# Kernel tuning notes

Hardware: AMD Instinct MI355X
Metric: run time of the kernel (lower is better)

The kernel has to match this reference:

```python
import jax, jax.numpy as jnp
import numpy as np

EPS_GAUSS = 1e-15
EPS_SOFTMAX = 1e-16

N, F, M, K = 200000, 256, 128, 8
ATT = 128
NUM_GRAPHS = 1024


def setup_inputs() -> dict:
    key = jax.random.key(0)
    ks = jax.random.split(key, 7)
    x = jax.random.normal(ks[0], (N, F), dtype=jnp.float32)
    # glorot-ish scales keep pre-gaussian activations in a sane range
    g = jax.random.normal(ks[1], (F, K * M), dtype=jnp.float32) * 0.05
    mu = jax.random.normal(ks[2], (K, M), dtype=jnp.float32) * 0.1
    sigma = jax.random.normal(ks[3], (K, M), dtype=jnp.float32) * 0.1
    w1 = jax.random.normal(ks[4], (ATT, M), dtype=jnp.float32) * 0.09
    w2 = jax.random.normal(ks[5], (1, ATT), dtype=jnp.float32) * 0.1
    batch = jnp.sort(jax.random.randint(ks[6], (N,), 0, NUM_GRAPHS, dtype=jnp.int64))
    return {"x": x, "g": g, "mu": mu, "sigma": sigma, "w1": w1,
            "w2": w2, "batch": batch, "num_graphs": NUM_GRAPHS}


def reference(x, g, mu, sigma, w1, w2, batch, num_graphs):
    n = x.shape[0]
    k, m = mu.shape
    # GMM "conv": dense matmul then Gaussian-mixture elementwise chain
    out = (x @ g).reshape(n, k, m)                       # [N, K, M]
    gauss = jnp.exp(-0.5 * (out - mu[None]) ** 2 / (EPS_GAUSS + sigma[None] ** 2))
    H = jnp.sum(out * gauss, axis=1)                     # [N, M]
    # attention pooling: scores per node
    a = jnp.tanh(H @ w1.T)                               # [N, ATT] (b1 unused in source)
    scores = a @ w2.T                                    # [N, 1]
    # segment (per-graph) softmax
    smax = jax.ops.segment_max(scores, batch, num_segments=num_graphs)
    e = jnp.exp(scores - smax[batch])
    ssum = jax.ops.segment_sum(e, batch, num_segments=num_graphs)
    S = e / (ssum[batch] + EPS_SOFTMAX)                  # [N, 1]
    # scatter_add pooling -> [num_graphs, M]
    return jax.ops.segment_sum(S * H, batch, num_segments=num_graphs)
```

## Files before the change

kernel.cpp:

```cpp
#include <hip/hip_runtime.h>
#include <hip/hip_bf16.h>
#include <hip/hip_fp16.h>
#include <math.h>

#define N_NODES 200000
#define FDIM    256
#define MDIM    128
#define KMIX    8
#define ATTD    128
#define NGRAPH  1024
#define TSN     64

typedef _Float16 half8 __attribute__((ext_vector_type(8)));
typedef _Float16 half4 __attribute__((ext_vector_type(4)));
typedef float    floatx4 __attribute__((ext_vector_type(4)));

__global__ __launch_bounds__(256) void pack_g(
    const float* __restrict__ g, _Float16* __restrict__ gh, _Float16* __restrict__ gl)
{
    int t    = blockIdx.x * 256 + threadIdx.x;
    int lane = t & 63;
    int frag = t >> 6;
    int fc   = frag & 7;
    int ctg  = (frag >> 3) & 7;
    int k    = frag >> 6;
    int col  = k * 128 + ctg * 16 + (lane & 15);
    int f0   = fc * 32 + (lane >> 4) * 8;
    half8 vh, vl;
    #pragma unroll
    for (int j = 0; j < 8; ++j) {
        float v = g[(size_t)(f0 + j) * 1024 + col];
        _Float16 h = (_Float16)v;
        vh[j] = h;
        vl[j] = (_Float16)(v - (float)h);
    }
    *(half8*)(gh + (size_t)t * 8) = vh;
    *(half8*)(gl + (size_t)t * 8) = vl;
}

__global__ __launch_bounds__(256) void pack_w1(
    const float* __restrict__ w1, _Float16* __restrict__ w1h, _Float16* __restrict__ w1l)
{
    int t    = blockIdx.x * 256 + threadIdx.x;
    int lane = t & 63;
    int frag = t >> 6;
    int mc   = frag & 3;
    int ctg  = frag >> 2;
    int att  = ctg * 16 + (lane & 15);
    int m0   = mc * 32 + (lane >> 4) * 8;
    half8 vh, vl;
    #pragma unroll
    for (int j = 0; j < 8; ++j) {
        float v = w1[att * MDIM + m0 + j];
        _Float16 h = (_Float16)v;
        vh[j] = h;
        vl[j] = (_Float16)(v - (float)h);
    }
    *(half8*)(w1h + (size_t)t * 8) = vh;
    *(half8*)(w1l + (size_t)t * 8) = vl;
}

__global__ __launch_bounds__(512, 4) void fused_forward(
    const float* __restrict__ x,
    const _Float16* __restrict__ gh, const _Float16* __restrict__ gl,
    const float* __restrict__ mu, const float* __restrict__ sigma,
    const _Float16* __restrict__ w1h, const _Float16* __restrict__ w1l,
    const float* __restrict__ w2,
    float* __restrict__ Hout, float* __restrict__ scores)
{
    __shared__ unsigned char smem[64 * 264 * 2 * 2];
    _Float16* xs_h = (_Float16*)smem;
    _Float16* xs_l = xs_h + 64 * 264;
    float*    Hs   = (float*)smem;
    float*    spart = (float*)(smem + 64 * 264 * 2);

    const int tid   = threadIdx.x;
    const int nBase = blockIdx.x * TSN;

    {
        const float4* xg = (const float4*)x;
        #pragma unroll
        for (int r = 0; r < 8; ++r) {
            int idx  = r * 512 + tid;
            int row  = idx >> 6;
            int quad = idx & 63;
            float4 v = xg[(size_t)(nBase + row) * 64 + quad];
            half4 h, l;
            h[0] = (_Float16)v.x; l[0] = (_Float16)(v.x - (float)h[0]);
            h[1] = (_Float16)v.y; l[1] = (_Float16)(v.y - (float)h[1]);
            h[2] = (_Float16)v.z; l[2] = (_Float16)(v.z - (float)h[2]);
            h[3] = (_Float16)v.w; l[3] = (_Float16)(v.w - (float)h[3]);
            *(half4*)&xs_h[row * 264 + quad * 4] = h;
            *(half4*)&xs_l[row * 264 + quad * 4] = l;
        }
    }
    __syncthreads();

    const int wave  = tid >> 6;
    const int lane  = tid & 63;
    const int c15   = lane & 15;
    const int q     = lane >> 4;
    const int nhalf = wave >> 2;
    const int colq  = wave & 3;

    float h[2][2][4];
    #pragma unroll
    for (int rt = 0; rt < 2; ++rt)
        #pragma unroll
        for (int ct = 0; ct < 2; ++ct)
            #pragma unroll
            for (int rg = 0; rg < 4; ++rg) h[rt][ct][rg] = 0.f;

    #pragma unroll 1
    for (int k = 0; k < KMIX; ++k) {
        floatx4 acc[2][2];
        #pragma unroll
        for (int rt = 0; rt < 2; ++rt)
            #pragma unroll
            for (int ct = 0; ct < 2; ++ct) acc[rt][ct] = (floatx4)0.f;

        #pragma unroll 2
        for (int fc = 0; fc < 8; ++fc) {
            const int f0 = fc * 32 + q * 8;
            half8 Ah[2], Al[2];
            #pragma unroll
            for (int rt = 0; rt < 2; ++rt) {
                int node = nhalf * 32 + rt * 16 + c15;
                Ah[rt] = *(const half8*)&xs_h[node * 264 + f0];
                Al[rt] = *(const half8*)&xs_l[node * 264 + f0];
            }
            half8 Bh[2], Bl[2];
            #pragma unroll
            for (int ct = 0; ct < 2; ++ct) {
                int ctg = colq * 2 + ct;
                size_t off = ((size_t)((k * 8 + ctg) * 8 + fc) * 64 + lane) * 8;
                Bh[ct] = *(const half8*)(gh + off);
                Bl[ct] = *(const half8*)(gl + off);
            }
            #pragma unroll
            for (int rt = 0; rt < 2; ++rt)
                #pragma unroll
                for (int ct = 0; ct < 2; ++ct) {
                    acc[rt][ct] = __builtin_amdgcn_mfma_f32_16x16x32_f16(Ah[rt], Bh[ct], acc[rt][ct], 0, 0, 0);
                    acc[rt][ct] = __builtin_amdgcn_mfma_f32_16x16x32_f16(Ah[rt], Bl[ct], acc[rt][ct], 0, 0, 0);
                    acc[rt][ct] = __builtin_amdgcn_mfma_f32_16x16x32_f16(Al[rt], Bh[ct], acc[rt][ct], 0, 0, 0);
                }
        }

        #pragma unroll
        for (int ct = 0; ct < 2; ++ct) {
            int col = k * 128 + colq * 32 + ct * 16 + c15;
            float muv = mu[col];
            float sg  = sigma[col];
            float iv  = 1.0f / (1e-15f + sg * sg);
            #pragma unroll
            for (int rt = 0; rt < 2; ++rt)
                #pragma unroll
                for (int rg = 0; rg < 4; ++rg) {
                    float o = acc[rt][ct][rg];
                    float d = o - muv;
                    h[rt][ct][rg] += o * __expf(-0.5f * d * d * iv);
                }
        }
    }

    __syncthreads();
    const int HS_LD = MDIM + 4;
    #pragma unroll
    for (int rt = 0; rt < 2; ++rt)
        #pragma unroll
        for (int ct = 0; ct < 2; ++ct)
            #pragma unroll
            for (int rg = 0; rg < 4; ++rg) {
                int n = nhalf * 32 + rt * 16 + q * 4 + rg;
                int m = colq * 32 + ct * 16 + c15;
                float v = h[rt][ct][rg];
                Hs[n * HS_LD + m] = v;
                Hout[(size_t)(nBase + n) * MDIM + m] = v;
            }
    __syncthreads();

    {
        floatx4 datt[2][2];
        #pragma unroll
        for (int rt = 0; rt < 2; ++rt)
            #pragma unroll
            for (int ct = 0; ct < 2; ++ct) datt[rt][ct] = (floatx4)0.f;

        #pragma unroll
        for (int mc = 0; mc < 4; ++mc) {
            half8 Ah[2], Al[2];
            #pragma unroll
            for (int rt = 0; rt < 2; ++rt) {
                int node = nhalf * 32 + rt * 16 + c15;
                const float* hp = &Hs[node * HS_LD + mc * 32 + q * 8];
                #pragma unroll
                for (int j = 0; j < 8; ++j) {
                    float v = hp[j];
                    _Float16 hi = (_Float16)v;
                    Ah[rt][j] = hi;
                    Al[rt][j] = (_Float16)(v - (float)hi);
                }
            }
            #pragma unroll
            for (int ct = 0; ct < 2; ++ct) {
                int frag = (colq * 2 + ct) * 4 + mc;
                size_t off = ((size_t)frag * 64 + lane) * 8;
                half8 Bh = *(const half8*)(w1h + off);
                half8 Bl = *(const half8*)(w1l + off);
                #pragma unroll
                for (int rt = 0; rt < 2; ++rt) {
                    datt[rt][ct] = __builtin_amdgcn_mfma_f32_16x16x32_f16(Ah[rt], Bh, datt[rt][ct], 0, 0, 0);
                    datt[rt][ct] = __builtin_amdgcn_mfma_f32_16x16x32_f16(Ah[rt], Bl, datt[rt][ct], 0, 0, 0);
                    datt[rt][ct] = __builtin_amdgcn_mfma_f32_16x16x32_f16(Al[rt], Bh, datt[rt][ct], 0, 0, 0);
                }
            }
        }

        float w2v[2];
        #pragma unroll
        for (int ct = 0; ct < 2; ++ct) w2v[ct] = w2[colq * 32 + ct * 16 + c15];

        #pragma unroll
        for (int rt = 0; rt < 2; ++rt) {
            #pragma unroll
            for (int rg = 0; rg < 4; ++rg) {
                float p = 0.f;
                #pragma unroll
                for (int ct = 0; ct < 2; ++ct) {
                    float dot = datt[rt][ct][rg];
                    float e2 = __expf(2.f * dot);
                    float av = 1.f - 2.f / (e2 + 1.f);
                    p = fmaf(av, w2v[ct], p);
                }
                p += __shfl_xor(p, 1);
                p += __shfl_xor(p, 2);
                p += __shfl_xor(p, 4);
                p += __shfl_xor(p, 8);
                if (c15 == 0) {
                    int n = nhalf * 32 + rt * 16 + q * 4 + rg;
                    spart[n * 4 + colq] = p;
                }
            }
        }
    }
    __syncthreads();
    if (tid < 64) {
        const float* sp = &spart[tid * 4];
        scores[nBase + tid] = (sp[0] + sp[1]) + (sp[2] + sp[3]);
    }
}

__global__ __launch_bounds__(256) void segment_pool(
    const float* __restrict__ H, const float* __restrict__ scores,
    const int* __restrict__ batch, float* __restrict__ out)
{
    const int gidx = blockIdx.x;
    const int tid  = threadIdx.x;

    int lo = 0, hi = N_NODES;
    while (lo < hi) { int mid = (lo + hi) >> 1; if (batch[mid] <  gidx) lo = mid + 1; else hi = mid; }
    const int start = lo;
    hi = N_NODES;
    while (lo < hi) { int mid = (lo + hi) >> 1; if (batch[mid] <= gidx) lo = mid + 1; else hi = mid; }
    const int end = lo;

    __shared__ float red[4];

    float mx = -INFINITY;
    for (int i = start + tid; i < end; i += 256) mx = fmaxf(mx, scores[i]);
    #pragma unroll
    for (int o = 32; o > 0; o >>= 1) mx = fmaxf(mx, __shfl_xor(mx, o));
    if ((tid & 63) == 0) red[tid >> 6] = mx;
    __syncthreads();
    mx = fmaxf(fmaxf(red[0], red[1]), fmaxf(red[2], red[3]));
    __syncthreads();

    float s = 0.f;
    for (int i = start + tid; i < end; i += 256) s += __expf(scores[i] - mx);
    #pragma unroll
    for (int o = 32; o > 0; o >>= 1) s += __shfl_xor(s, o);
    if ((tid & 63) == 0) red[tid >> 6] = s;
    __syncthreads();
    s = red[0] + red[1] + red[2] + red[3];
    const float inv = 1.f / (s + 1e-16f);

    const int m = tid & 127;
    const int p = tid >> 7;
    float acc = 0.f;
    for (int i = start + p; i < end; i += 2)
        acc = fmaf(__expf(scores[i] - mx), H[(size_t)i * MDIM + m], acc);
    __shared__ float part[2][128];
    part[p][m] = acc;
    __syncthreads();
    if (tid < 128) out[gidx * MDIM + tid] = (part[0][tid] + part[1][tid]) * inv;
}

extern "C" void kernel_launch(void* const* d_in, const int* in_sizes, int n_in,
                              void* d_out, int out_size, void* d_ws, size_t ws_size,
                              hipStream_t stream)
{
    const float* x     = (const float*)d_in[0];
    const float* g     = (const float*)d_in[1];
    const float* mu    = (const float*)d_in[2];
    const float* sigma = (const float*)d_in[3];
    const float* w1    = (const float*)d_in[4];
    const float* w2    = (const float*)d_in[5];
    const int*   batch = (const int*)d_in[6];
    float* out = (float*)d_out;

    float*    H      = (float*)d_ws;
    float*    scores = H + (size_t)N_NODES * MDIM;
    _Float16* ghp    = (_Float16*)(scores + N_NODES);
    _Float16* glp    = ghp + (size_t)FDIM * KMIX * MDIM;
    _Float16* w1hp   = glp + (size_t)FDIM * KMIX * MDIM;
    _Float16* w1lp   = w1hp + (size_t)ATTD * MDIM;

    pack_g<<<128, 256, 0, stream>>>(g, ghp, glp);
    pack_w1<<<8, 256, 0, stream>>>(w1, w1hp, w1lp);
    fused_forward<<<N_NODES / TSN, 512, 0, stream>>>(x, ghp, glp, mu, sigma,
                                                     w1hp, w1lp, w2, H, scores);
    segment_pool<<<NGRAPH, 256, 0, stream>>>(H, scores, batch, out);
}
```

Before: 680.9 us.

## Double-buffer GEMM operand loads, coalesce H stores, restructure segment pooling

The main GEMM loop now software-pipelines its LDS A-fragment and global B-fragment loads into double-buffered registers, prefetching the next k/fc step while the current MFMAs run. H is staged through shared memory and written to global with coalesced float4 stores instead of scattered scalar writes. The segment pooling kernel fuses the exp-sum pass with the weighted accumulation, caching exp values in shared-memory chunks and reading H as float4 across 8 node-parallel groups. This adds register pressure from the doubled operand buffers, which could hurt occupancy at launch bounds of 512 threads and 4 blocks.

```diff
diff --git a/kernel.cpp b/kernel.cpp
--- a/kernel.cpp
+++ b/kernel.cpp
@@ -68,11 +68,11 @@
     const float* __restrict__ w2,
     float* __restrict__ Hout, float* __restrict__ scores)
 {
-    __shared__ unsigned char smem[64 * 264 * 2 * 2];
+    __shared__ unsigned char smem[64 * 264 * 2 * 2 + 512];
     _Float16* xs_h = (_Float16*)smem;
     _Float16* xs_l = xs_h + 64 * 264;
     float*    Hs   = (float*)smem;
-    float*    spart = (float*)(smem + 64 * 264 * 2);
+    float*    spart = (float*)(smem + 64 * 264 * 2 * 2);
 
     const int tid   = threadIdx.x;
     const int nBase = blockIdx.x * TSN;
@@ -103,6 +103,9 @@
     const int nhalf = wave >> 2;
     const int colq  = wave & 3;
 
+    const _Float16* gh0 = gh + (size_t)(colq * 2) * 4096 + lane * 8;
+    const _Float16* gl0 = gl + (size_t)(colq * 2) * 4096 + lane * 8;
+
     float h[2][2][4];
     #pragma unroll
     for (int rt = 0; rt < 2; ++rt)
@@ -110,6 +113,31 @@
         for (int ct = 0; ct < 2; ++ct)
             #pragma unroll
             for (int rg = 0; rg < 4; ++rg) h[rt][ct][rg] = 0.f;
+
+    half8 Ah[2][2], Al[2][2], Bh[2][2], Bl[2][2];
+
+#define LOAD_A(buf, fcv)                                                      \
+    {                                                                         \
+        const int f0_ = (fcv) * 32 + q * 8;                                   \
+        _Pragma("unroll")                                                     \
+        for (int rt = 0; rt < 2; ++rt) {                                      \
+            int node_ = nhalf * 32 + rt * 16 + c15;                           \
+            Ah[buf][rt] = *(const half8*)&xs_h[node_ * 264 + f0_];            \
+            Al[buf][rt] = *(const half8*)&xs_l[node_ * 264 + f0_];            \
+        }                                                                     \
+    }
+#define LOAD_B(buf, kv, fcv)                                                  \
+    {                                                                         \
+        size_t o_ = (size_t)(kv) * 32768 + (size_t)(fcv) * 512;               \
+        _Pragma("unroll")                                                     \
+        for (int ct = 0; ct < 2; ++ct) {                                      \
+            Bh[buf][ct] = *(const half8*)(gh0 + o_ + ct * 4096);              \
+            Bl[buf][ct] = *(const half8*)(gl0 + o_ + ct * 4096);              \
+        }                                                                     \
+    }
+
+    LOAD_A(0, 0)
+    LOAD_B(0, 0, 0)
 
     #pragma unroll 1
     for (int k = 0; k < KMIX; ++k) {
@@ -119,31 +147,20 @@
             #pragma unroll
             for (int ct = 0; ct < 2; ++ct) acc[rt][ct] = (floatx4)0.f;
 
-        #pragma unroll 2
+        #pragma unroll
         for (int fc = 0; fc < 8; ++fc) {
-            const int f0 = fc * 32 + q * 8;
-            half8 Ah[2], Al[2];
-            #pragma unroll
-            for (int rt = 0; rt < 2; ++rt) {
-                int node = nhalf * 32 + rt * 16 + c15;
-                Ah[rt] = *(const half8*)&xs_h[node * 264 + f0];
-                Al[rt] = *(const half8*)&xs_l[node * 264 + f0];
-            }
-            half8 Bh[2], Bl[2];
-            #pragma unroll
-            for (int ct = 0; ct < 2; ++ct) {
-                int ctg = colq * 2 + ct;
-                size_t off = ((size_t)((k * 8 + ctg) * 8 + fc) * 64 + lane) * 8;
-                Bh[ct] = *(const half8*)(gh + off);
-                Bl[ct] = *(const half8*)(gl + off);
-            }
+            const int cur = fc & 1, nxt = cur ^ 1;
+            const int nfc = (fc + 1) & 7;
+            const int nk  = (fc == 7) ? ((k + 1) & 7) : k;
+            LOAD_A(nxt, nfc)
+            LOAD_B(nxt, nk, nfc)
             #pragma unroll
             for (int rt = 0; rt < 2; ++rt)
                 #pragma unroll
                 for (int ct = 0; ct < 2; ++ct) {
-                    acc[rt][ct] = __builtin_amdgcn_mfma_f32_16x16x32_f16(Ah[rt], Bh[ct], acc[rt][ct], 0, 0, 0);
-                    acc[rt][ct] = __builtin_amdgcn_mfma_f32_16x16x32_f16(Ah[rt], Bl[ct], acc[rt][ct], 0, 0, 0);
-                    acc[rt][ct] = __builtin_amdgcn_mfma_f32_16x16x32_f16(Al[rt], Bh[ct], acc[rt][ct], 0, 0, 0);
+                    acc[rt][ct] = __builtin_amdgcn_mfma_f32_16x16x32_f16(Ah[cur][rt], Bh[cur][ct], acc[rt][ct], 0, 0, 0);
+                    acc[rt][ct] = __builtin_amdgcn_mfma_f32_16x16x32_f16(Ah[cur][rt], Bl[cur][ct], acc[rt][ct], 0, 0, 0);
+                    acc[rt][ct] = __builtin_amdgcn_mfma_f32_16x16x32_f16(Al[cur][rt], Bh[cur][ct], acc[rt][ct], 0, 0, 0);
                 }
         }
 
@@ -163,6 +180,8 @@
                 }
         }
     }
+#undef LOAD_A
+#undef LOAD_B
 
     __syncthreads();
     const int HS_LD = MDIM + 4;
@@ -174,11 +193,18 @@
             for (int rg = 0; rg < 4; ++rg) {
                 int n = nhalf * 32 + rt * 16 + q * 4 + rg;
                 int m = colq * 32 + ct * 16 + c15;
-                float v = h[rt][ct][rg];
-                Hs[n * HS_LD + m] = v;
-                Hout[(size_t)(nBase + n) * MDIM + m] = v;
+                Hs[n * HS_LD + m] = h[rt][ct][rg];
             }
     __syncthreads();
+
+    #pragma unroll
+    for (int r = 0; r < 4; ++r) {
+        int idx  = r * 512 + tid;
+        int node = idx >> 5;
+        int mq   = idx & 31;
+        float4 v = *(const float4*)&Hs[node * HS_LD + mq * 4];
+        *(float4*)&Hout[(size_t)(nBase + node) * MDIM + mq * 4] = v;
+    }
 
     {
         floatx4 datt[2][2];
@@ -189,7 +215,7 @@
 
         #pragma unroll
         for (int mc = 0; mc < 4; ++mc) {
-            half8 Ah[2], Al[2];
+            half8 Ahh[2], All[2];
             #pragma unroll
             for (int rt = 0; rt < 2; ++rt) {
                 int node = nhalf * 32 + rt * 16 + c15;
@@ -198,21 +224,21 @@
                 for (int j = 0; j < 8; ++j) {
                     float v = hp[j];
                     _Float16 hi = (_Float16)v;
-                    Ah[rt][j] = hi;
-                    Al[rt][j] = (_Float16)(v - (float)hi);
+                    Ahh[rt][j] = hi;
+                    All[rt][j] = (_Float16)(v - (float)hi);
                 }
             }
             #pragma unroll
             for (int ct = 0; ct < 2; ++ct) {
                 int frag = (colq * 2 + ct) * 4 + mc;
                 size_t off = ((size_t)frag * 64 + lane) * 8;
-                half8 Bh = *(const half8*)(w1h + off);
-                half8 Bl = *(const half8*)(w1l + off);
+                half8 Bhh = *(const half8*)(w1h + off);
+                half8 Bll = *(const half8*)(w1l + off);
                 #pragma unroll
                 for (int rt = 0; rt < 2; ++rt) {
-                    datt[rt][ct] = __builtin_amdgcn_mfma_f32_16x16x32_f16(Ah[rt], Bh, datt[rt][ct], 0, 0, 0);
-                    datt[rt][ct] = __builtin_amdgcn_mfma_f32_16x16x32_f16(Ah[rt], Bl, datt[rt][ct], 0, 0, 0);
-                    datt[rt][ct] = __builtin_amdgcn_mfma_f32_16x16x32_f16(Al[rt], Bh, datt[rt][ct], 0, 0, 0);
+                    datt[rt][ct] = __builtin_amdgcn_mfma_f32_16x16x32_f16(Ahh[rt], Bhh, datt[rt][ct], 0, 0, 0);
+                    datt[rt][ct] = __builtin_amdgcn_mfma_f32_16x16x32_f16(Ahh[rt], Bll, datt[rt][ct], 0, 0, 0);
+                    datt[rt][ct] = __builtin_amdgcn_mfma_f32_16x16x32_f16(All[rt], Bhh, datt[rt][ct], 0, 0, 0);
                 }
             }
         }
@@ -251,6 +277,7 @@
     }
 }
 
+#define CHUNK 1024
 __global__ __launch_bounds__(256) void segment_pool(
     const float* __restrict__ H, const float* __restrict__ scores,
     const int* __restrict__ batch, float* __restrict__ out)
@@ -266,6 +293,8 @@
     const int end = lo;
 
     __shared__ float red[4];
+    __shared__ float ebuf[CHUNK];
+    __shared__ float part[8][MDIM];
 
     float mx = -INFINITY;
     for (int i = start + tid; i < end; i += 256) mx = fmaxf(mx, scores[i]);
@@ -274,26 +303,47 @@
     if ((tid & 63) == 0) red[tid >> 6] = mx;
     __syncthreads();
     mx = fmaxf(fmaxf(red[0], red[1]), fmaxf(red[2], red[3]));
-    __syncthreads();
-
-    float s = 0.f;
-    for (int i = start + tid; i < end; i += 256) s += __expf(scores[i] - mx);
-    #pragma unroll
-    for (int o = 32; o > 0; o >>= 1) s += __shfl_xor(s, o);
-    if ((tid & 63) == 0) red[tid >> 6] = s;
-    __syncthreads();
-    s = red[0] + red[1] + red[2] + red[3];
-    const float inv = 1.f / (s + 1e-16f);
-
-    const int m = tid & 127;
-    const int p = tid >> 7;
-    float acc = 0.f;
-    for (int i = start + p; i < end; i += 2)
-        acc = fmaf(__expf(scores[i] - mx), H[(size_t)i * MDIM + m], acc);
-    __shared__ float part[2][128];
-    part[p][m] = acc;
-    __syncthreads();
-    if (tid < 128) out[gidx * MDIM + tid] = (part[0][tid] + part[1][tid]) * inv;
+
+    const int mq = tid & 31;
+    const int p  = tid >> 5;
+    float4 acc = make_float4(0.f, 0.f, 0.f, 0.f);
+    float ls = 0.f;
+
+    for (int c0 = start; c0 < end; c0 += CHUNK) {
+        const int clen = min(end - c0, CHUNK);
+        __syncthreads();
+        for (int i = tid; i < clen; i += 256) {
+            float e = __expf(scores[c0 + i] - mx);
+            ebuf[i] = e;
+            ls += e;
+        }
+        __syncthreads();
+        for (int i = p; i < clen; i += 8) {
+            float e = ebuf[i];
+            const float4 hv = *(const float4*)&H[(size_t)(c0 + i) * MDIM + mq * 4];
+            acc.x = fmaf(e, hv.x, acc.x);
+            acc.y = fmaf(e, hv.y, acc.y);
+            acc.z = fmaf(e, hv.z, acc.z);
+            acc.w = fmaf(e, hv.w, acc.w);
+        }
+    }
+
+    #pragma unroll
+    for (int o = 32; o > 0; o >>= 1) ls += __shfl_xor(ls, o);
+    if ((tid & 63) == 0) red[tid >> 6] = ls;
+    part[p][mq * 4 + 0] = acc.x;
+    part[p][mq * 4 + 1] = acc.y;
+    part[p][mq * 4 + 2] = acc.z;
+    part[p][mq * 4 + 3] = acc.w;
+    __syncthreads();
+    if (tid < MDIM) {
+        float s = red[0] + red[1] + red[2] + red[3];
+        const float inv = 1.f / (s + 1e-16f);
+        float a = 0.f;
+        #pragma unroll
+        for (int pp = 0; pp < 8; ++pp) a += part[pp][tid];
+        out[gidx * MDIM + tid] = a * inv;
+    }
 }
 
 extern "C" void kernel_launch(void* const* d_in, const int* in_sizes, int n_in,
```

New measurement: 1.133 ms. +66.4%, slower.
